# Kernel optimization log

Measured on AMD Instinct MI355X. Metric: run time of the kernel, lower is better.

The kernel has to match this reference:

```python
import jax, jax.numpy as jnp
import numpy as np

N = 256      # max_num_nodes (padded nodes per graph)
H = 8        # attention heads
F = 128      # feature_dim
L = 9        # n_layers
INFLA = 6.0  # MCL inflation
EPS = 1e-6


def _layernorm(x, g, b):
    mu = x.mean(-1, keepdims=True)
    var = ((x - mu) ** 2).mean(-1, keepdims=True)
    return (x - mu) / jnp.sqrt(var + 1e-5) * g + b


def _get_mcl(adj):
    # Markov-cluster style power iteration with inflation every 3rd step (num=6)
    m = adj / (adj.sum(-1, keepdims=True) + EPS)
    r = m
    for i in range(6):
        r = m @ r
        if (i + 1) % 3 == 0:
            r = r ** INFLA
        r = r / (r.sum(-1, keepdims=True) + EPS)
    return r


def _forward(input_x, edge_attr, gcn_lin_w, gcn_root_emb, gcn_edge_w,
             gcn_norm_g, gcn_norm_b, ln_in_g, ln_in_b, ln_ffn_g, ln_ffn_b,
             mcl_w, q_w, k_w, v_w, merge_w, merge_b,
             ffn_w1, ffn_b1, ffn_w2, ffn_b2, final_g, final_b,
             edge_index, n_counts, root):
    BN = input_x.shape[0]
    B = BN // N
    dh = F // H
    row, col = edge_index[0], edge_index[1]

    # --- adjacency / padding masks (built once, as in GC_T.forward) ---
    valid = jnp.arange(N)[None, :] < n_counts[:, None]                    # [B,N]
    eb, es, et = row // N, row % N, col % N
    adj = jnp.zeros((B, N, N), bool).at[eb, es, et].set(True)
    adj = adj | (jnp.eye(N, dtype=bool)[None] & valid[:, :, None])        # self loops on valid nodes
    pad = ~(valid[:, :, None] & valid[:, None, :])
    pad_bias = jnp.where(pad, -1024.0, 0.0)[..., None]                    # [B,N,N,1] (broadcast over H)
    mcl = _get_mcl(adj.astype(input_x.dtype))[..., None]                  # [B,N,N,1]

    # --- GCN degree normalization (degree of row index, +1) ---
    deg = jnp.zeros((BN,), input_x.dtype).at[row].add(1.0) + 1.0
    dis = deg ** -0.5
    enorm = (dis[row] * dis[col])[:, None]                                # [E,1]

    out = input_x.reshape(B, N, F)
    for i in range(L):
        # ---- GCNConv: gather-relu-scatter message passing ----
        res = out
        h = out.reshape(BN, F) @ gcn_lin_w[i].T                           # [BN,F]
        ee = edge_attr @ gcn_edge_w[i].T                                  # [E,F]
        msg = enorm * jax.nn.relu(h[row] + ee)                            # x_j = x[row]
        agg = jax.ops.segment_sum(msg, col, num_segments=BN)              # aggregate at target
        g = agg + jax.nn.relu(h + gcn_root_emb[i][root]) / deg[:, None]
        g = jax.nn.relu(_layernorm(g, gcn_norm_g[i], gcn_norm_b[i]))
        out = g.reshape(B, N, F) + res

        # ---- Encoder: biased multi-head attention + FFN ----
        bias4 = (pad_bias + mcl * mcl_w[i][:, 0]).transpose(0, 3, 1, 2)   # [B,H,N,N]
        x = out
        q = (x @ q_w[i].T).reshape(B, N, H, dh).transpose(0, 2, 1, 3) * (dh ** -0.5)
        k = (x @ k_w[i].T).reshape(B, N, H, dh).transpose(0, 2, 1, 3)
        v = (x @ v_w[i].T).reshape(B, N, H, dh).transpose(0, 2, 1, 3)
        att = jax.nn.softmax(jnp.einsum('bhnd,bhmd->bhnm', q, k) + bias4, axis=-1)
        o = jnp.einsum('bhnm,bhmd->bhnd', att, v).transpose(0, 2, 1, 3).reshape(B, N, F)
        o = o @ merge_w[i].T + merge_b[i]
        x = _layernorm(o + x, ln_in_g[i], ln_in_b[i])
        f = jax.nn.gelu(x @ ffn_w1[i].T + ffn_b1[i], approximate=False)
        f = f @ ffn_w2[i].T + ffn_b2[i]
        out = _layernorm(x + f, ln_ffn_g[i], ln_ffn_b[i])

    return _layernorm(out, final_g, final_b)


def setup_inputs() -> dict:
    key = jax.random.key(0)
    ks = jax.random.split(key, 16)
    B, E = 16, 65536
    s = 0.02 * L ** -0.5
    w = lambda k, shape: jax.random.normal(k, shape, jnp.float32) * s
    return {
        'input_x': jax.random.normal(ks[0], (B * N, F), jnp.float32),
        'edge_attr': jax.random.normal(ks[1], (E, 7), jnp.float32),
        'gcn_lin_w': w(ks[2], (L, F, F)),
        'gcn_root_emb': jax.random.normal(ks[3], (L, 2, F), jnp.float32) * 0.02,
        'gcn_edge_w': w(ks[4], (L, F, 7)),
        'gcn_norm_g': jnp.ones((L, F), jnp.float32),
        'gcn_norm_b': jnp.zeros((L, F), jnp.float32),
        'ln_in_g': jnp.ones((L, F), jnp.float32),
        'ln_in_b': jnp.zeros((L, F), jnp.float32),
        'ln_ffn_g': jnp.ones((L, F), jnp.float32),
        'ln_ffn_b': jnp.zeros((L, F), jnp.float32),
        'mcl_w': w(ks[5], (L, H, 1)),
        'q_w': w(ks[6], (L, F, F)),
        'k_w': w(ks[7], (L, F, F)),
        'v_w': w(ks[8], (L, F, F)),
        'merge_w': w(ks[9], (L, F, F)),
        'merge_b': jnp.zeros((L, F), jnp.float32),
        'ffn_w1': w(ks[10], (L, 2 * F, F)),
        'ffn_b1': jnp.zeros((L, 2 * F), jnp.float32),
        'ffn_w2': w(ks[11], (L, F, 2 * F)),
        'ffn_b2': jnp.zeros((L, F), jnp.float32),
        'final_g': jnp.ones((F,), jnp.float32),
        'final_b': jnp.zeros((F,), jnp.float32),
        'edge_index': jax.random.randint(ks[12], (2, E), 0, B * N),
        'n_counts': jax.random.randint(ks[13], (B,), 1, N + 1),
        'root': jax.random.randint(ks[14], (B * N,), 0, 2),
    }


def reference(input_x, edge_attr, gcn_lin_w, gcn_root_emb, gcn_edge_w,
              gcn_norm_g, gcn_norm_b, ln_in_g, ln_in_b, ln_ffn_g, ln_ffn_b,
              mcl_w, q_w, k_w, v_w, merge_w, merge_b,
              ffn_w1, ffn_b1, ffn_w2, ffn_b2, final_g, final_b,
              edge_index, n_counts, root):
    return _forward(input_x, edge_attr, gcn_lin_w, gcn_root_emb, gcn_edge_w,
                    gcn_norm_g, gcn_norm_b, ln_in_g, ln_in_b, ln_ffn_g, ln_ffn_b,
                    mcl_w, q_w, k_w, v_w, merge_w, merge_b,
                    ffn_w1, ffn_b1, ffn_w2, ffn_b2, final_g, final_b,
                    edge_index, n_counts, root)
```

## Files before the change

kernel.cpp:

```cpp
#include <hip/hip_runtime.h>
#include <hip/hip_bf16.h>
#include <math.h>

#define NLAYER 9

typedef unsigned short u16;
typedef __attribute__((ext_vector_type(8))) short short8;
typedef __attribute__((ext_vector_type(4))) float f32x4;

__device__ inline u16 f2bf(float x) {
  unsigned int u = __float_as_uint(x);
  unsigned int r = (u + 0x7fffu + ((u >> 16) & 1u)) >> 16;
  return (u16)r;
}
__device__ inline float gelu_exact(float x) {
  return 0.5f * x * (1.0f + erff(x * 0.7071067811865476f));
}

__global__ void setup1_kernel(const int* __restrict__ ei, float* __restrict__ adj,
                              float* __restrict__ deg, int* __restrict__ ccount, int E, int EB,
                              const float* __restrict__ s0, const float* __restrict__ s1,
                              const float* __restrict__ s2, const float* __restrict__ s3,
                              const float* __restrict__ s4, const float* __restrict__ s5,
                              const float* __restrict__ s6, u16* __restrict__ d0,
                              u16* __restrict__ d1, u16* __restrict__ d2,
                              u16* __restrict__ d3, u16* __restrict__ d4,
                              u16* __restrict__ d5, u16* __restrict__ d6) {
  int bid = blockIdx.x;
  if (bid < EB) {
    int e = bid * 256 + threadIdx.x;
    if (e >= E) return;
    int r = ei[e], c = ei[E + e];
    int b = r >> 8;
    adj[((size_t)b << 16) + ((size_t)(r & 255) << 8) + (c & 255)] = 1.0f;
    atomicAdd(&deg[r], 1.0f);
    atomicAdd(&ccount[c], 1);
  } else {
    int idx = bid - EB;
    int f = idx / 72, cb = idx % 72;
    const float* s;
    u16* d;
    int n;
    switch (f) {
      case 0: s = s0; d = d0; n = NLAYER * 4096; break;
      case 1: s = s1; d = d1; n = NLAYER * 4096; break;
      case 2: s = s2; d = d2; n = NLAYER * 4096; break;
      case 3: s = s3; d = d3; n = NLAYER * 4096; break;
      case 4: s = s4; d = d4; n = NLAYER * 4096; break;
      case 5: s = s5; d = d5; n = NLAYER * 8192; break;
      default: s = s6; d = d6; n = NLAYER * 8192; break;
    }
    for (int i = cb * 256 + threadIdx.x; i < n; i += 72 * 256) {
      float4 v = ((const float4*)s)[i];
      u16 p4[4] = {f2bf(v.x), f2bf(v.y), f2bf(v.z), f2bf(v.w)};
      ((ushort4*)d)[i] = *(ushort4*)p4;
    }
  }
}

__global__ __launch_bounds__(1024) void setup2_kernel(const int* __restrict__ nc,
                                                      float* __restrict__ adj,
                                                      float* __restrict__ deg,
                                                      float* __restrict__ dis,
                                                      const int* __restrict__ ccount,
                                                      int* __restrict__ rowptr, int BN) {
  int bid = blockIdx.x;
  int t = threadIdx.x;
  if (bid < (BN >> 10)) {
    int n = bid * 1024 + t;
    int b = n >> 8, i = n & 255;
    if (i < nc[b]) adj[((size_t)b << 16) + ((size_t)i << 8) + i] = 1.0f;
    float d = deg[n] + 1.0f;
    deg[n] = d;
    dis[n] = rsqrtf(d);
  } else {
    __shared__ int part[1024];
    int base = t * 4;
    int c[4], s = 0;
#pragma unroll
    for (int i = 0; i < 4; i++) { c[i] = (base + i < BN) ? ccount[base + i] : 0; s += c[i]; }
    part[t] = s;
    __syncthreads();
    for (int o = 1; o < 1024; o <<= 1) {
      int v = (t >= o) ? part[t - o] : 0;
      __syncthreads();
      part[t] += v;
      __syncthreads();
    }
    int excl = part[t] - s;
#pragma unroll
    for (int i = 0; i < 4; i++) {
      if (base + i < BN) rowptr[base + i] = excl;
      excl += c[i];
    }
    if (t == 1023) rowptr[BN] = part[1023];
  }
}

__global__ __launch_bounds__(256) void setup3_kernel(float* __restrict__ m,
                                                     const int* __restrict__ ei,
                                                     const float* __restrict__ dis,
                                                     const int* __restrict__ rowptr,
                                                     int* __restrict__ fill,
                                                     int* __restrict__ src_s,
                                                     int* __restrict__ eidx_s,
                                                     float* __restrict__ enorm_s, int E,
                                                     int BN) {
  int bid = blockIdx.x;
  int w = threadIdx.x >> 6, lane = threadIdx.x & 63;
  if (bid < (BN >> 2)) {
    int row = bid * 4 + w;
    float4 v4 = *(const float4*)(m + (size_t)row * 256 + lane * 4);
    float s = v4.x + v4.y + v4.z + v4.w;
#pragma unroll
    for (int o = 32; o > 0; o >>= 1) s += __shfl_xor(s, o, 64);
    float inv = 1.f / (s + 1e-6f);
    v4.x *= inv;
    v4.y *= inv;
    v4.z *= inv;
    v4.w *= inv;
    *(float4*)(m + (size_t)row * 256 + lane * 4) = v4;
  } else {
    int e = (bid - (BN >> 2)) * 256 + threadIdx.x;
    if (e >= E) return;
    int r = ei[e], c = ei[E + e];
    int pos = rowptr[c] + atomicAdd(&fill[c], 1);
    src_s[pos] = r;
    eidx_s[pos] = e;
    enorm_s[pos] = dis[r] * dis[c];
  }
}

__global__ __launch_bounds__(256) void mcl_prep_kernel(const float* __restrict__ m,
                                                       u16* __restrict__ mb,
                                                       u16* __restrict__ rT) {
  int b = blockIdx.z;
  const float* M = m + ((size_t)b << 16);
  u16* MB = mb + ((size_t)b << 16);
  u16* RT = rT + ((size_t)b << 16);
  int r0 = blockIdx.x * 64, c0 = blockIdx.y * 64;
  __shared__ float ts[64][65];
  int t = threadIdx.x;
  int i = t >> 2, jb = (t & 3) * 16;
#pragma unroll
  for (int g = 0; g < 4; g++) {
    int j = jb + g * 4;
    float4 v = *(const float4*)(M + (size_t)(r0 + i) * 256 + c0 + j);
    ts[i][j] = v.x; ts[i][j + 1] = v.y; ts[i][j + 2] = v.z; ts[i][j + 3] = v.w;
    u16 p4[4] = {f2bf(v.x), f2bf(v.y), f2bf(v.z), f2bf(v.w)};
    *(ushort4*)(MB + (size_t)(r0 + i) * 256 + c0 + j) = *(ushort4*)p4;
  }
  __syncthreads();
#pragma unroll
  for (int g = 0; g < 4; g++) {
    int j = jb + g * 4;
    u16 p4[4] = {f2bf(ts[j][i]), f2bf(ts[j + 1][i]), f2bf(ts[j + 2][i]), f2bf(ts[j + 3][i])};
    *(ushort4*)(RT + (size_t)(c0 + i) * 256 + r0 + j) = *(ushort4*)p4;
  }
}

__global__ __launch_bounds__(256) void mcl_iter_kernel(const u16* __restrict__ rT,
                                                       const u16* __restrict__ mb,
                                                       u16* __restrict__ rTn,
                                                       float* __restrict__ mclr,
                                                       int inflate, int fin) {
  __shared__ float red[64];
  int b = blockIdx.x >> 4, i0 = (blockIdx.x & 15) * 16;
  int w = threadIdx.x >> 6, lane = threadIdx.x & 63;
  int m16 = lane & 15, quad = lane >> 4;
  const u16* A = rT + ((size_t)b << 16);
  const u16* Bm = mb + ((size_t)b << 16);
  f32x4 acc[4];
#pragma unroll
  for (int tj = 0; tj < 4; tj++) acc[tj] = (f32x4){0.f, 0.f, 0.f, 0.f};
  for (int k0 = 0; k0 < 256; k0 += 32) {
    short8 bb = *(const short8*)(Bm + (size_t)(i0 + m16) * 256 + k0 + quad * 8);
#pragma unroll
    for (int tj = 0; tj < 4; tj++) {
      short8 a = *(const short8*)(A + (size_t)(w * 64 + tj * 16 + m16) * 256 + k0 + quad * 8);
      acc[tj] = __builtin_amdgcn_mfma_f32_16x16x32_bf16(a, bb, acc[tj], 0, 0, 0);
    }
  }
  float ps = 0.f;
#pragma unroll
  for (int tj = 0; tj < 4; tj++)
#pragma unroll
    for (int reg = 0; reg < 4; reg++) {
      float v = acc[tj][reg];
      if (inflate) { float v2 = v * v; v = v2 * v2 * v2; }
      acc[tj][reg] = v;
      ps += v;
    }
  ps += __shfl_xor(ps, 16, 64);
  ps += __shfl_xor(ps, 32, 64);
  if (quad == 0) red[w * 16 + m16] = ps;
  __syncthreads();
  float tot = red[m16] + red[16 + m16] + red[32 + m16] + red[48 + m16];
  float inv = 1.f / (tot + 1e-6f);
  if (fin) {
    float* dst = mclr + ((size_t)b << 16);
#pragma unroll
    for (int tj = 0; tj < 4; tj++)
#pragma unroll
      for (int reg = 0; reg < 4; reg++) {
        int j = w * 64 + tj * 16 + quad * 4 + reg;
        dst[(size_t)(i0 + m16) * 256 + j] = acc[tj][reg] * inv;
      }
  } else {
    u16* dst = rTn + ((size_t)b << 16);
#pragma unroll
    for (int tj = 0; tj < 4; tj++)
#pragma unroll
      for (int reg = 0; reg < 4; reg++) {
        int j = w * 64 + tj * 16 + quad * 4 + reg;
        dst[(size_t)j * 256 + i0 + m16] = f2bf(acc[tj][reg] * inv);
      }
  }
}

__global__ __launch_bounds__(256) void copyx_lin_kernel(const float* __restrict__ x,
                                                        const u16* __restrict__ wlin0,
                                                        float* __restrict__ outb,
                                                        float* __restrict__ hbuf) {
  __shared__ u16 st[16 * 136];
  int m0 = blockIdx.x * 16;
  int tid = threadIdx.x;
  int w = tid >> 6, lane = tid & 63;
  int m16 = lane & 15, quad = lane >> 4;
  for (int i = tid; i < 2048; i += 256) {
    int row = i >> 7, col = i & 127;
    float v = x[(size_t)(m0 + row) * 128 + col];
    outb[(size_t)(m0 + row) * 128 + col] = v;
    st[row * 136 + col] = f2bf(v);
  }
  __syncthreads();
  int c0 = w * 32;
  f32x4 acc[2] = {{0.f, 0.f, 0.f, 0.f}, {0.f, 0.f, 0.f, 0.f}};
#pragma unroll
  for (int k0 = 0; k0 < 128; k0 += 32) {
    short8 a = *(const short8*)(st + m16 * 136 + k0 + quad * 8);
#pragma unroll
    for (int t = 0; t < 2; t++) {
      short8 bb = *(const short8*)(wlin0 + (size_t)(c0 + t * 16 + m16) * 128 + k0 + quad * 8);
      acc[t] = __builtin_amdgcn_mfma_f32_16x16x32_bf16(a, bb, acc[t], 0, 0, 0);
    }
  }
#pragma unroll
  for (int t = 0; t < 2; t++)
#pragma unroll
    for (int reg = 0; reg < 4; reg++)
      hbuf[(size_t)(m0 + quad * 4 + reg) * 128 + c0 + t * 16 + m16] = acc[t][reg];
}

__global__ __launch_bounds__(256) void gcn_ln_kernel(
    const int* __restrict__ rowptr, const int* __restrict__ src_s,
    const int* __restrict__ eidx_s, const float* __restrict__ enorm_s,
    const float* __restrict__ ea, const float* __restrict__ We, const float* __restrict__ h,
    const float* __restrict__ remb, const int* __restrict__ root,
    const float* __restrict__ deg, const float* __restrict__ gamma,
    const float* __restrict__ beta, float* __restrict__ out, u16* __restrict__ out16) {
  __shared__ float Wt[7 * 128];
  for (int idx = threadIdx.x; idx < 896; idx += 256) {
    int f = idx & 127, k = idx >> 7;
    Wt[k * 128 + f] = We[f * 7 + k];
  }
  __syncthreads();
  int n = blockIdx.x * 4 + (threadIdx.x >> 6);
  int lane = threadIdx.x & 63;
  int f0 = lane, f1 = lane + 64;
  int p0 = rowptr[n], p1 = rowptr[n + 1];
  float a0 = 0.f, a1 = 0.f;
  int r = 0, e = 0;
  float en = 0.f;
  if (p0 < p1) { r = src_s[p0]; e = eidx_s[p0]; en = enorm_s[p0]; }
  for (int p = p0; p < p1; p++) {
    int rn = 0, enx = 0;
    float ennx = 0.f;
    if (p + 1 < p1) { rn = src_s[p + 1]; enx = eidx_s[p + 1]; ennx = enorm_s[p + 1]; }
    const float* eae = ea + (size_t)e * 7;
    float h0 = h[(size_t)r * 128 + f0];
    float h1 = h[(size_t)r * 128 + f1];
    float d0 = 0.f, d1 = 0.f;
#pragma unroll
    for (int k = 0; k < 7; k++) {
      float ev = eae[k];
      d0 += ev * Wt[k * 128 + f0];
      d1 += ev * Wt[k * 128 + f1];
    }
    a0 += en * fmaxf(h0 + d0, 0.f);
    a1 += en * fmaxf(h1 + d1, 0.f);
    r = rn; e = enx; en = ennx;
  }
  float invd = 1.0f / deg[n];
  const float* re = remb + root[n] * 128;
  size_t base = (size_t)n * 128;
  float g0 = a0 + fmaxf(h[base + f0] + re[f0], 0.f) * invd;
  float g1 = a1 + fmaxf(h[base + f1] + re[f1], 0.f) * invd;
  float s = g0 + g1, ss = g0 * g0 + g1 * g1;
#pragma unroll
  for (int o = 32; o > 0; o >>= 1) { s += __shfl_xor(s, o, 64); ss += __shfl_xor(ss, o, 64); }
  float mu = s * 0.0078125f;
  float var = ss * 0.0078125f - mu * mu;
  float rs = rsqrtf(var + 1e-5f);
  float y0 = fmaxf((g0 - mu) * rs * gamma[f0] + beta[f0], 0.f) + out[base + f0];
  float y1 = fmaxf((g1 - mu) * rs * gamma[f1] + beta[f1], 0.f) + out[base + f1];
  out[base + f0] = y0;
  out[base + f1] = y1;
  out16[base + f0] = f2bf(y0);
  out16[base + f1] = f2bf(y1);
}

__global__ __launch_bounds__(256) void attn_qkv_kernel(
    const u16* __restrict__ x16, const u16* __restrict__ wq, const u16* __restrict__ wk,
    const u16* __restrict__ wv, const float* __restrict__ mclr,
    const float* __restrict__ mclw, const int* __restrict__ ncnt, u16* __restrict__ o) {
  __shared__ float ks[256][16];
  __shared__ float vs[256][16];
  __shared__ float qs[64][16];
  int qt = blockIdx.x, hh = blockIdx.y, b = blockIdx.z;
  int t = threadIdx.x;
  int w = t >> 6, lane = t & 63;
  int m16 = lane & 15, quad = lane >> 4;
  const u16* bk = wk + (size_t)(hh * 16 + m16) * 128 + quad * 8;
  const u16* bv = wv + (size_t)(hh * 16 + m16) * 128 + quad * 8;
#pragma unroll
  for (int tj = 0; tj < 4; tj++) {
    int rb = w * 64 + tj * 16;
    const u16* arow = x16 + (size_t)(b * 256 + rb + m16) * 128 + quad * 8;
    f32x4 ak = {0.f, 0.f, 0.f, 0.f}, av = {0.f, 0.f, 0.f, 0.f};
#pragma unroll
    for (int k0 = 0; k0 < 128; k0 += 32) {
      short8 a = *(const short8*)(arow + k0);
      ak = __builtin_amdgcn_mfma_f32_16x16x32_bf16(a, *(const short8*)(bk + k0), ak, 0, 0, 0);
      av = __builtin_amdgcn_mfma_f32_16x16x32_bf16(a, *(const short8*)(bv + k0), av, 0, 0, 0);
    }
#pragma unroll
    for (int reg = 0; reg < 4; reg++) {
      ks[rb + quad * 4 + reg][m16] = ak[reg];
      vs[rb + quad * 4 + reg][m16] = av[reg];
    }
  }
  {
    const u16* bq = wq + (size_t)(hh * 16 + m16) * 128 + quad * 8;
    const u16* arow = x16 + (size_t)(b * 256 + qt * 64 + w * 16 + m16) * 128 + quad * 8;
    f32x4 aq = {0.f, 0.f, 0.f, 0.f};
#pragma unroll
    for (int k0 = 0; k0 < 128; k0 += 32) {
      short8 a = *(const short8*)(arow + k0);
      aq = __builtin_amdgcn_mfma_f32_16x16x32_bf16(a, *(const short8*)(bq + k0), aq, 0, 0, 0);
    }
#pragma unroll
    for (int reg = 0; reg < 4; reg++) qs[w * 16 + quad * 4 + reg][m16] = aq[reg] * 0.25f;
  }
  __syncthreads();
  int i = qt * 64 + (t >> 2);
  int d0 = (t & 3) * 4;
  int nc = ncnt[b];
  bool vi = i < nc;
  float wh = mclw[hh];
  float qv[4] = {qs[t >> 2][d0], qs[t >> 2][d0 + 1], qs[t >> 2][d0 + 2], qs[t >> 2][d0 + 3]};
  const float* mrow = mclr + ((size_t)(b * 256 + i)) * 256;
  float acc[4] = {0.f, 0.f, 0.f, 0.f};
  float lsum = 0.f;
  for (int j0 = 0; j0 < 256; j0 += 4) {
    float4 mc = *(const float4*)(mrow + j0);
    float mcv[4] = {mc.x, mc.y, mc.z, mc.w};
#pragma unroll
    for (int jj = 0; jj < 4; jj++) {
      int j = j0 + jj;
      float s = qv[0] * ks[j][d0] + qv[1] * ks[j][d0 + 1] + qv[2] * ks[j][d0 + 2] +
                qv[3] * ks[j][d0 + 3];
      s += __shfl_xor(s, 1, 64);
      s += __shfl_xor(s, 2, 64);
      float bias = mcv[jj] * wh + ((vi && j >= nc) ? -1024.f : 0.f);
      float pe = __expf(s + bias);
      lsum += pe;
      acc[0] += pe * vs[j][d0];
      acc[1] += pe * vs[j][d0 + 1];
      acc[2] += pe * vs[j][d0 + 2];
      acc[3] += pe * vs[j][d0 + 3];
    }
  }
  float inv = 1.f / lsum;
  u16 p4[4] = {f2bf(acc[0] * inv), f2bf(acc[1] * inv), f2bf(acc[2] * inv), f2bf(acc[3] * inv)};
  *(ushort4*)(o + ((size_t)(b * 256 + i) * 128 + hh * 16 + d0)) = *(ushort4*)p4;
}

__global__ __launch_bounds__(256) void merge_ffn_kernel(
    const u16* __restrict__ ob16, const u16* __restrict__ Wm, const float* __restrict__ mb,
    const float* __restrict__ gam1, const float* __restrict__ bet1,
    const u16* __restrict__ W1, const float* __restrict__ b1, const u16* __restrict__ W2,
    const float* __restrict__ b2, const float* __restrict__ gam2,
    const float* __restrict__ bet2, float* __restrict__ outb,
    const u16* __restrict__ wlin_next, float* __restrict__ hbuf,
    const float* __restrict__ fing, const float* __restrict__ finb) {
  __shared__ float redS[64], redSS[64];
  __shared__ u16 st[16 * 136];
  __shared__ u16 f1s[16 * 264];
  int tid = threadIdx.x;
  int w = tid >> 6, lane = tid & 63;
  int m16 = lane & 15, quad = lane >> 4;
  int m0 = blockIdx.x * 16;
  f32x4 acc[2] = {{0.f, 0.f, 0.f, 0.f}, {0.f, 0.f, 0.f, 0.f}};
  {
    const u16* arow = ob16 + (size_t)(m0 + m16) * 128 + quad * 8;
#pragma unroll
    for (int k0 = 0; k0 < 128; k0 += 32) {
      short8 a = *(const short8*)(arow + k0);
#pragma unroll
      for (int t = 0; t < 2; t++) {
        short8 bb = *(const short8*)(Wm + (size_t)(w * 32 + t * 16 + m16) * 128 + k0 + quad * 8);
        acc[t] = __builtin_amdgcn_mfma_f32_16x16x32_bf16(a, bb, acc[t], 0, 0, 0);
      }
    }
  }
  float s4[4] = {0.f, 0.f, 0.f, 0.f}, ss4[4] = {0.f, 0.f, 0.f, 0.f};
#pragma unroll
  for (int t = 0; t < 2; t++) {
    int col = w * 32 + t * 16 + m16;
    float bi = mb[col];
#pragma unroll
    for (int reg = 0; reg < 4; reg++) {
      int row = m0 + quad * 4 + reg;
      float v = acc[t][reg] + bi + outb[(size_t)row * 128 + col];
      acc[t][reg] = v;
      s4[reg] += v;
      ss4[reg] += v * v;
    }
  }
#pragma unroll
  for (int o = 1; o <= 8; o <<= 1)
#pragma unroll
    for (int reg = 0; reg < 4; reg++) {
      s4[reg] += __shfl_xor(s4[reg], o, 64);
      ss4[reg] += __shfl_xor(ss4[reg], o, 64);
    }
  if (m16 == 0) {
#pragma unroll
    for (int reg = 0; reg < 4; reg++) {
      redS[w * 16 + quad * 4 + reg] = s4[reg];
      redSS[w * 16 + quad * 4 + reg] = ss4[reg];
    }
  }
  __syncthreads();
  float mu[4], rsd[4];
#pragma unroll
  for (int reg = 0; reg < 4; reg++) {
    int r = quad * 4 + reg;
    float S = redS[r] + redS[16 + r] + redS[32 + r] + redS[48 + r];
    float SS = redSS[r] + redSS[16 + r] + redSS[32 + r] + redSS[48 + r];
    mu[reg] = S * 0.0078125f;
    float var = SS * 0.0078125f - mu[reg] * mu[reg];
    rsd[reg] = rsqrtf(var + 1e-5f);
  }
  float xr[2][4];
#pragma unroll
  for (int t = 0; t < 2; t++) {
    int col = w * 32 + t * 16 + m16;
    float g = gam1[col], be = bet1[col];
#pragma unroll
    for (int reg = 0; reg < 4; reg++) {
      float y = (acc[t][reg] - mu[reg]) * rsd[reg] * g + be;
      xr[t][reg] = y;
      st[(quad * 4 + reg) * 136 + col] = f2bf(y);
    }
  }
  __syncthreads();
  {
    f32x4 acc1[4];
#pragma unroll
    for (int t = 0; t < 4; t++) acc1[t] = (f32x4){0.f, 0.f, 0.f, 0.f};
#pragma unroll
    for (int k0 = 0; k0 < 128; k0 += 32) {
      short8 a = *(const short8*)(st + m16 * 136 + k0 + quad * 8);
#pragma unroll
      for (int t = 0; t < 4; t++) {
        short8 bb = *(const short8*)(W1 + (size_t)(w * 64 + t * 16 + m16) * 128 + k0 + quad * 8);
        acc1[t] = __builtin_amdgcn_mfma_f32_16x16x32_bf16(a, bb, acc1[t], 0, 0, 0);
      }
    }
#pragma unroll
    for (int t = 0; t < 4; t++) {
      int col = w * 64 + t * 16 + m16;
      float bi = b1[col];
#pragma unroll
      for (int reg = 0; reg < 4; reg++)
        f1s[(quad * 4 + reg) * 264 + col] = f2bf(gelu_exact(acc1[t][reg] + bi));
    }
  }
  __syncthreads();
#pragma unroll
  for (int t = 0; t < 2; t++) acc[t] = (f32x4){0.f, 0.f, 0.f, 0.f};
#pragma unroll
  for (int k0 = 0; k0 < 256; k0 += 32) {
    short8 a = *(const short8*)(f1s + m16 * 264 + k0 + quad * 8);
#pragma unroll
    for (int t = 0; t < 2; t++) {
      short8 bb = *(const short8*)(W2 + (size_t)(w * 32 + t * 16 + m16) * 256 + k0 + quad * 8);
      acc[t] = __builtin_amdgcn_mfma_f32_16x16x32_bf16(a, bb, acc[t], 0, 0, 0);
    }
  }
#pragma unroll
  for (int reg = 0; reg < 4; reg++) { s4[reg] = 0.f; ss4[reg] = 0.f; }
#pragma unroll
  for (int t = 0; t < 2; t++) {
    int col = w * 32 + t * 16 + m16;
    float bi = b2[col];
#pragma unroll
    for (int reg = 0; reg < 4; reg++) {
      float v = acc[t][reg] + bi + xr[t][reg];
      acc[t][reg] = v;
      s4[reg] += v;
      ss4[reg] += v * v;
    }
  }
#pragma unroll
  for (int o = 1; o <= 8; o <<= 1)
#pragma unroll
    for (int reg = 0; reg < 4; reg++) {
      s4[reg] += __shfl_xor(s4[reg], o, 64);
      ss4[reg] += __shfl_xor(ss4[reg], o, 64);
    }
  __syncthreads();
  if (m16 == 0) {
#pragma unroll
    for (int reg = 0; reg < 4; reg++) {
      redS[w * 16 + quad * 4 + reg] = s4[reg];
      redSS[w * 16 + quad * 4 + reg] = ss4[reg];
    }
  }
  __syncthreads();
#pragma unroll
  for (int reg = 0; reg < 4; reg++) {
    int r = quad * 4 + reg;
    float S = redS[r] + redS[16 + r] + redS[32 + r] + redS[48 + r];
    float SS = redSS[r] + redSS[16 + r] + redSS[32 + r] + redSS[48 + r];
    mu[reg] = S * 0.0078125f;
    float var = SS * 0.0078125f - mu[reg] * mu[reg];
    rsd[reg] = rsqrtf(var + 1e-5f);
  }
#pragma unroll
  for (int t = 0; t < 2; t++) {
    int col = w * 32 + t * 16 + m16;
    float g = gam2[col], be = bet2[col];
#pragma unroll
    for (int reg = 0; reg < 4; reg++)
      acc[t][reg] = (acc[t][reg] - mu[reg]) * rsd[reg] * g + be;
  }
  if (fing) {
    float s2[4] = {0.f, 0.f, 0.f, 0.f}, ss2[4] = {0.f, 0.f, 0.f, 0.f};
#pragma unroll
    for (int t = 0; t < 2; t++)
#pragma unroll
      for (int reg = 0; reg < 4; reg++) {
        float v = acc[t][reg];
        s2[reg] += v;
        ss2[reg] += v * v;
      }
#pragma unroll
    for (int o = 1; o <= 8; o <<= 1)
#pragma unroll
      for (int reg = 0; reg < 4; reg++) {
        s2[reg] += __shfl_xor(s2[reg], o, 64);
        ss2[reg] += __shfl_xor(ss2[reg], o, 64);
      }
    __syncthreads();
    if (m16 == 0) {
#pragma unroll
      for (int reg = 0; reg < 4; reg++) {
        redS[w * 16 + quad * 4 + reg] = s2[reg];
        redSS[w * 16 + quad * 4 + reg] = ss2[reg];
      }
    }
    __syncthreads();
#pragma unroll
    for (int reg = 0; reg < 4; reg++) {
      int r = quad * 4 + reg;
      float S = redS[r] + redS[16 + r] + redS[32 + r] + redS[48 + r];
      float SS = redSS[r] + redSS[16 + r] + redSS[32 + r] + redSS[48 + r];
      mu[reg] = S * 0.0078125f;
      float var = SS * 0.0078125f - mu[reg] * mu[reg];
      rsd[reg] = rsqrtf(var + 1e-5f);
    }
#pragma unroll
    for (int t = 0; t < 2; t++) {
      int col = w * 32 + t * 16 + m16;
      float g = fing[col], be = finb[col];
#pragma unroll
      for (int reg = 0; reg < 4; reg++) {
        int row = m0 + quad * 4 + reg;
        outb[(size_t)row * 128 + col] = (acc[t][reg] - mu[reg]) * rsd[reg] * g + be;
      }
    }
    return;
  }
#pragma unroll
  for (int t = 0; t < 2; t++) {
    int col = w * 32 + t * 16 + m16;
#pragma unroll
    for (int reg = 0; reg < 4; reg++) {
      int row = m0 + quad * 4 + reg;
      float y = acc[t][reg];
      outb[(size_t)row * 128 + col] = y;
      st[(quad * 4 + reg) * 136 + col] = f2bf(y);
    }
  }
  __syncthreads();
  {
    f32x4 acc2[2] = {{0.f, 0.f, 0.f, 0.f}, {0.f, 0.f, 0.f, 0.f}};
#pragma unroll
    for (int k0 = 0; k0 < 128; k0 += 32) {
      short8 a = *(const short8*)(st + m16 * 136 + k0 + quad * 8);
#pragma unroll
      for (int t = 0; t < 2; t++) {
        short8 bb =
            *(const short8*)(wlin_next + (size_t)(w * 32 + t * 16 + m16) * 128 + k0 + quad * 8);
        acc2[t] = __builtin_amdgcn_mfma_f32_16x16x32_bf16(a, bb, acc2[t], 0, 0, 0);
      }
    }
#pragma unroll
    for (int t = 0; t < 2; t++)
#pragma unroll
      for (int reg = 0; reg < 4; reg++)
        hbuf[(size_t)(m0 + quad * 4 + reg) * 128 + w * 32 + t * 16 + m16] = acc2[t][reg];
  }
}

extern "C" void kernel_launch(void* const* d_in, const int* in_sizes, int n_in,
                              void* d_out, int out_size, void* d_ws, size_t ws_size,
                              hipStream_t stream) {
  const float* input_x = (const float*)d_in[0];
  const float* edge_attr = (const float*)d_in[1];
  const float* gcn_lin_w = (const float*)d_in[2];
  const float* gcn_root = (const float*)d_in[3];
  const float* gcn_edge_w = (const float*)d_in[4];
  const float* gcn_ng = (const float*)d_in[5];
  const float* gcn_nb = (const float*)d_in[6];
  const float* ln_in_g = (const float*)d_in[7];
  const float* ln_in_b = (const float*)d_in[8];
  const float* ln_ffn_g = (const float*)d_in[9];
  const float* ln_ffn_b = (const float*)d_in[10];
  const float* mcl_w = (const float*)d_in[11];
  const float* q_w = (const float*)d_in[12];
  const float* k_w = (const float*)d_in[13];
  const float* v_w = (const float*)d_in[14];
  const float* merge_w = (const float*)d_in[15];
  const float* merge_b = (const float*)d_in[16];
  const float* ffn_w1 = (const float*)d_in[17];
  const float* ffn_b1 = (const float*)d_in[18];
  const float* ffn_w2 = (const float*)d_in[19];
  const float* ffn_b2 = (const float*)d_in[20];
  const float* final_g = (const float*)d_in[21];
  const float* final_b = (const float*)d_in[22];
  const int* edge_index = (const int*)d_in[23];
  const int* n_counts = (const int*)d_in[24];
  const int* root = (const int*)d_in[25];

  const int E = in_sizes[23] / 2;
  const int B = in_sizes[24];
  const int BN = B * 256;
  const int EB = (E + 255) / 256;

  float* ws = (float*)d_ws;
  size_t off = 0;
  auto alloc = [&](size_t n) {
    off = (off + 3) & ~(size_t)3;
    float* q = ws + off;
    off += n;
    return q;
  };
  const size_t NN2 = (size_t)B * 256 * 256;
  const size_t XF = (size_t)BN * 128;
  float* mclr = alloc(NN2);
  float* mbuf = alloc(NN2);
  float* hbuf = alloc(XF);
  float* deg = alloc(BN);
  int* ccount = (int*)alloc(BN);
  int* fill = (int*)alloc(BN);
  float* dis = alloc(BN);
  int* rowptr = (int*)alloc(BN + 1);
  int* src_s = (int*)alloc(E);
  int* eidx_s = (int*)alloc(E);
  float* enorm_s = alloc(E);
  u16* mb16 = (u16*)alloc(NN2 / 2);
  u16* rT16 = (u16*)alloc(NN2 / 2);
  u16* cT16 = (u16*)alloc(NN2 / 2);
  u16* ob16 = (u16*)alloc(XF / 2);
  u16* outb16 = (u16*)alloc(XF / 2);
  u16* wlin16 = (u16*)alloc((size_t)NLAYER * 8192);
  u16* wq16 = (u16*)alloc((size_t)NLAYER * 8192);
  u16* wk16 = (u16*)alloc((size_t)NLAYER * 8192);
  u16* wv16 = (u16*)alloc((size_t)NLAYER * 8192);
  u16* wm16 = (u16*)alloc((size_t)NLAYER * 8192);
  u16* wf116 = (u16*)alloc((size_t)NLAYER * 16384);
  u16* wf216 = (u16*)alloc((size_t)NLAYER * 16384);
  float* outb = (float*)d_out;

  hipMemsetAsync(mbuf, 0, NN2 * sizeof(float), stream);
  hipMemsetAsync(deg, 0, 3 * BN * sizeof(float), stream);
  setup1_kernel<<<EB + 504, 256, 0, stream>>>(edge_index, mbuf, deg, ccount, E, EB, gcn_lin_w,
                                              q_w, k_w, v_w, merge_w, ffn_w1, ffn_w2, wlin16,
                                              wq16, wk16, wv16, wm16, wf116, wf216);
  setup2_kernel<<<BN / 1024 + 1, 1024, 0, stream>>>(n_counts, mbuf, deg, dis, ccount, rowptr,
                                                    BN);
  setup3_kernel<<<BN / 4 + EB, 256, 0, stream>>>(mbuf, edge_index, dis, rowptr, fill, src_s,
                                                 eidx_s, enorm_s, E, BN);
  dim3 mmg(4, 4, B);
  mcl_prep_kernel<<<mmg, 256, 0, stream>>>(mbuf, mb16, rT16);
  {
    u16 *cur = rT16, *nxt = cT16;
    for (int it = 0; it < 6; it++) {
      int inflate = (it == 2 || it == 5) ? 1 : 0;
      mcl_iter_kernel<<<16 * B, 256, 0, stream>>>(cur, mb16, nxt, mclr, inflate,
                                                  it == 5 ? 1 : 0);
      u16* tmp = cur;
      cur = nxt;
      nxt = tmp;
    }
  }
  copyx_lin_kernel<<<BN / 16, 256, 0, stream>>>(input_x, wlin16, outb, hbuf);

  dim3 ag(4, 8, B);
  for (int l = 0; l < NLAYER; l++) {
    gcn_ln_kernel<<<BN / 4, 256, 0, stream>>>(
        rowptr, src_s, eidx_s, enorm_s, edge_attr, gcn_edge_w + (size_t)l * 896, hbuf,
        gcn_root + (size_t)l * 256, root, deg, gcn_ng + l * 128, gcn_nb + l * 128, outb,
        outb16);
    attn_qkv_kernel<<<ag, 256, 0, stream>>>(outb16, wq16 + (size_t)l * 16384,
                                            wk16 + (size_t)l * 16384,
                                            wv16 + (size_t)l * 16384, mclr, mcl_w + l * 8,
                                            n_counts, ob16);
    const u16* wnext = (l + 1 < NLAYER) ? (wlin16 + (size_t)(l + 1) * 16384) : wlin16;
    const float* fg = (l == NLAYER - 1) ? final_g : nullptr;
    const float* fb = (l == NLAYER - 1) ? final_b : nullptr;
    merge_ffn_kernel<<<BN / 16, 256, 0, stream>>>(
        ob16, wm16 + (size_t)l * 16384, merge_b + l * 128, ln_in_g + l * 128,
        ln_in_b + l * 128, wf116 + (size_t)l * 32768, ffn_b1 + l * 256,
        wf216 + (size_t)l * 32768, ffn_b2 + l * 128, ln_ffn_g + l * 128, ln_ffn_b + l * 128,
        outb, wnext, hbuf, fg, fb);
  }
}
```

Before: 822.4 us.

## Split GCN edge loop across two waves per node and defer row normalization

The GCN message-passing kernel now assigns two wavefronts per destination node, each taking alternating edges, and combines the two partial sums through shared memory before the LayerNorm epilogue. The next neighbor's h row is prefetched one iteration ahead. Separately, setup3 no longer rewrites the normalized adjacency; it stores per-row inverse sums, which mcl_prep applies on load, removing one full read-write pass over the NxN matrices. The cost is twice as many blocks, an extra __syncthreads, and half the waves sitting idle during the epilogue.

Result: faster. 762.5 us (-7.3%).

```diff
diff --git a/kernel.cpp b/kernel.cpp
--- a/kernel.cpp
+++ b/kernel.cpp
@@ -97,7 +97,8 @@
   }
 }
 
-__global__ __launch_bounds__(256) void setup3_kernel(float* __restrict__ m,
+__global__ __launch_bounds__(256) void setup3_kernel(const float* __restrict__ m,
+                                                     float* __restrict__ rsinv,
                                                      const int* __restrict__ ei,
                                                      const float* __restrict__ dis,
                                                      const int* __restrict__ rowptr,
@@ -114,12 +115,7 @@
     float s = v4.x + v4.y + v4.z + v4.w;
 #pragma unroll
     for (int o = 32; o > 0; o >>= 1) s += __shfl_xor(s, o, 64);
-    float inv = 1.f / (s + 1e-6f);
-    v4.x *= inv;
-    v4.y *= inv;
-    v4.z *= inv;
-    v4.w *= inv;
-    *(float4*)(m + (size_t)row * 256 + lane * 4) = v4;
+    if (lane == 0) rsinv[row] = 1.f / (s + 1e-6f);
   } else {
     int e = (bid - (BN >> 2)) * 256 + threadIdx.x;
     if (e >= E) return;
@@ -132,6 +128,7 @@
 }
 
 __global__ __launch_bounds__(256) void mcl_prep_kernel(const float* __restrict__ m,
+                                                       const float* __restrict__ rsinv,
                                                        u16* __restrict__ mb,
                                                        u16* __restrict__ rT) {
   int b = blockIdx.z;
@@ -142,10 +139,12 @@
   __shared__ float ts[64][65];
   int t = threadIdx.x;
   int i = t >> 2, jb = (t & 3) * 16;
+  float riv = rsinv[(b << 8) + r0 + i];
 #pragma unroll
   for (int g = 0; g < 4; g++) {
     int j = jb + g * 4;
     float4 v = *(const float4*)(M + (size_t)(r0 + i) * 256 + c0 + j);
+    v.x *= riv; v.y *= riv; v.z *= riv; v.w *= riv;
     ts[i][j] = v.x; ts[i][j + 1] = v.y; ts[i][j + 2] = v.z; ts[i][j + 3] = v.w;
     u16 p4[4] = {f2bf(v.x), f2bf(v.y), f2bf(v.z), f2bf(v.w)};
     *(ushort4*)(MB + (size_t)(r0 + i) * 256 + c0 + j) = *(ushort4*)p4;
@@ -260,26 +259,39 @@
     const float* __restrict__ deg, const float* __restrict__ gamma,
     const float* __restrict__ beta, float* __restrict__ out, u16* __restrict__ out16) {
   __shared__ float Wt[7 * 128];
+  __shared__ float part[2][2][128];
   for (int idx = threadIdx.x; idx < 896; idx += 256) {
     int f = idx & 127, k = idx >> 7;
     Wt[k * 128 + f] = We[f * 7 + k];
   }
   __syncthreads();
-  int n = blockIdx.x * 4 + (threadIdx.x >> 6);
-  int lane = threadIdx.x & 63;
+  int w = threadIdx.x >> 6, lane = threadIdx.x & 63;
+  int nodeSlot = w >> 1, wv = w & 1;
+  int n = blockIdx.x * 2 + nodeSlot;
   int f0 = lane, f1 = lane + 64;
   int p0 = rowptr[n], p1 = rowptr[n + 1];
   float a0 = 0.f, a1 = 0.f;
+  int p = p0 + wv;
   int r = 0, e = 0;
-  float en = 0.f;
-  if (p0 < p1) { r = src_s[p0]; e = eidx_s[p0]; en = enorm_s[p0]; }
-  for (int p = p0; p < p1; p++) {
-    int rn = 0, enx = 0;
-    float ennx = 0.f;
-    if (p + 1 < p1) { rn = src_s[p + 1]; enx = eidx_s[p + 1]; ennx = enorm_s[p + 1]; }
+  float en = 0.f, h0 = 0.f, h1 = 0.f;
+  if (p < p1) {
+    r = src_s[p];
+    e = eidx_s[p];
+    en = enorm_s[p];
+    h0 = h[(size_t)r * 128 + f0];
+    h1 = h[(size_t)r * 128 + f1];
+  }
+  for (; p < p1; p += 2) {
+    int enx = 0;
+    float ennx = 0.f, hn0 = 0.f, hn1 = 0.f;
+    if (p + 2 < p1) {
+      int rn = src_s[p + 2];
+      enx = eidx_s[p + 2];
+      ennx = enorm_s[p + 2];
+      hn0 = h[(size_t)rn * 128 + f0];
+      hn1 = h[(size_t)rn * 128 + f1];
+    }
     const float* eae = ea + (size_t)e * 7;
-    float h0 = h[(size_t)r * 128 + f0];
-    float h1 = h[(size_t)r * 128 + f1];
     float d0 = 0.f, d1 = 0.f;
 #pragma unroll
     for (int k = 0; k < 7; k++) {
@@ -289,25 +301,38 @@
     }
     a0 += en * fmaxf(h0 + d0, 0.f);
     a1 += en * fmaxf(h1 + d1, 0.f);
-    r = rn; e = enx; en = ennx;
-  }
-  float invd = 1.0f / deg[n];
-  const float* re = remb + root[n] * 128;
-  size_t base = (size_t)n * 128;
-  float g0 = a0 + fmaxf(h[base + f0] + re[f0], 0.f) * invd;
-  float g1 = a1 + fmaxf(h[base + f1] + re[f1], 0.f) * invd;
-  float s = g0 + g1, ss = g0 * g0 + g1 * g1;
-#pragma unroll
-  for (int o = 32; o > 0; o >>= 1) { s += __shfl_xor(s, o, 64); ss += __shfl_xor(ss, o, 64); }
-  float mu = s * 0.0078125f;
-  float var = ss * 0.0078125f - mu * mu;
-  float rs = rsqrtf(var + 1e-5f);
-  float y0 = fmaxf((g0 - mu) * rs * gamma[f0] + beta[f0], 0.f) + out[base + f0];
-  float y1 = fmaxf((g1 - mu) * rs * gamma[f1] + beta[f1], 0.f) + out[base + f1];
-  out[base + f0] = y0;
-  out[base + f1] = y1;
-  out16[base + f0] = f2bf(y0);
-  out16[base + f1] = f2bf(y1);
+    e = enx;
+    en = ennx;
+    h0 = hn0;
+    h1 = hn1;
+  }
+  part[nodeSlot][wv][lane] = a0;
+  part[nodeSlot][wv][64 + lane] = a1;
+  __syncthreads();
+  if (wv == 0) {
+    a0 = part[nodeSlot][0][lane] + part[nodeSlot][1][lane];
+    a1 = part[nodeSlot][0][64 + lane] + part[nodeSlot][1][64 + lane];
+    float invd = 1.0f / deg[n];
+    const float* re = remb + root[n] * 128;
+    size_t base = (size_t)n * 128;
+    float g0 = a0 + fmaxf(h[base + f0] + re[f0], 0.f) * invd;
+    float g1 = a1 + fmaxf(h[base + f1] + re[f1], 0.f) * invd;
+    float s = g0 + g1, ss = g0 * g0 + g1 * g1;
+#pragma unroll
+    for (int o = 32; o > 0; o >>= 1) {
+      s += __shfl_xor(s, o, 64);
+      ss += __shfl_xor(ss, o, 64);
+    }
+    float mu = s * 0.0078125f;
+    float var = ss * 0.0078125f - mu * mu;
+    float rs = rsqrtf(var + 1e-5f);
+    float y0 = fmaxf((g0 - mu) * rs * gamma[f0] + beta[f0], 0.f) + out[base + f0];
+    float y1 = fmaxf((g1 - mu) * rs * gamma[f1] + beta[f1], 0.f) + out[base + f1];
+    out[base + f0] = y0;
+    out[base + f1] = y1;
+    out16[base + f0] = f2bf(y0);
+    out16[base + f1] = f2bf(y1);
+  }
 }
 
 __global__ __launch_bounds__(256) void attn_qkv_kernel(
@@ -678,6 +703,7 @@
   int* ccount = (int*)alloc(BN);
   int* fill = (int*)alloc(BN);
   float* dis = alloc(BN);
+  float* rsinv = alloc(BN);
   int* rowptr = (int*)alloc(BN + 1);
   int* src_s = (int*)alloc(E);
   int* eidx_s = (int*)alloc(E);
@@ -703,10 +729,10 @@
                                               wq16, wk16, wv16, wm16, wf116, wf216);
   setup2_kernel<<<BN / 1024 + 1, 1024, 0, stream>>>(n_counts, mbuf, deg, dis, ccount, rowptr,
                                                     BN);
-  setup3_kernel<<<BN / 4 + EB, 256, 0, stream>>>(mbuf, edge_index, dis, rowptr, fill, src_s,
-                                                 eidx_s, enorm_s, E, BN);
+  setup3_kernel<<<BN / 4 + EB, 256, 0, stream>>>(mbuf, rsinv, edge_index, dis, rowptr, fill,
+                                                 src_s, eidx_s, enorm_s, E, BN);
   dim3 mmg(4, 4, B);
-  mcl_prep_kernel<<<mmg, 256, 0, stream>>>(mbuf, mb16, rT16);
+  mcl_prep_kernel<<<mmg, 256, 0, stream>>>(mbuf, rsinv, mb16, rT16);
   {
     u16 *cur = rT16, *nxt = cT16;
     for (int it = 0; it < 6; it++) {
@@ -722,7 +748,7 @@
 
   dim3 ag(4, 8, B);
   for (int l = 0; l < NLAYER; l++) {
-    gcn_ln_kernel<<<BN / 4, 256, 0, stream>>>(
+    gcn_ln_kernel<<<BN / 2, 256, 0, stream>>>(
         rowptr, src_s, eidx_s, enorm_s, edge_attr, gcn_edge_w + (size_t)l * 896, hbuf,
         gcn_root + (size_t)l * 256, root, deg, gcn_ng + l * 128, gcn_nb + l * 128, outb,
         outb16);
```
